# Performance work log

Hardware: AMD Instinct MI355X
Metric: run time of the kernel (lower is better)

The kernel has to match this reference:

```python
import jax, jax.numpy as jnp
import numpy as np


def setup_inputs() -> dict:
    key = jax.random.key(0)
    k1, k2, k3 = jax.random.split(key, 3)
    num, c_in, c_out, din, dout = 64, 4, 4, 2, 2
    sx = sy = 256
    nx, ny = sx // 2 + sx % 2, sy // 2 + sy % 2
    x = jax.random.normal(k1, (num, c_in, din, sx, sy), dtype=jnp.float32)
    # weight tensor: (c_in, c_out, nx, ny, din, din, din, din, dout)
    tensors = jax.random.normal(k2, (c_in, c_out, nx, ny, din, din, din, din, dout), dtype=jnp.float32)
    bias = jax.random.normal(k3, (c_out, nx, ny, dout), dtype=jnp.float32) * 1e-8
    return {"x": x, "tensors": tensors, "bias": bias}


def reference(x, tensors, bias):
    # x: (n, c, d, sx, sy); tensors: (c, p, nx, ny, d, d, d, d, o); bias: (p, nx, ny, o)
    n, c, d, sx, sy = x.shape
    nx = sx // 2 + sx % 2
    ny = sy // 2 + sy % 2
    # boundary-clamped 2x2 patch indices (matches min(2*i+1, s-1) in the source)
    ix0 = jnp.arange(nx) * 2
    ix1 = jnp.minimum(ix0 + 1, sx - 1)
    iy0 = jnp.arange(ny) * 2
    iy1 = jnp.minimum(iy0 + 1, sy - 1)
    # four corner pixels of every 2x2 patch, each (n, c, d, nx, ny)
    a = x[:, :, :, ix0][:, :, :, :, iy0]  # (2i,   2j)
    b = x[:, :, :, ix1][:, :, :, :, iy0]  # (2i+1, 2j)
    e = x[:, :, :, ix0][:, :, :, :, iy1]  # (2i,   2j+1)
    f = x[:, :, :, ix1][:, :, :, :, iy1]  # (2i+1, 2j+1)
    # outer product of the four local features -> (n, c, nx, ny, d^4)
    patch = jnp.einsum('ncixy,ncjxy,nckxy,nclxy->ncxyijkl', a, b, e, f)
    patch = patch.reshape(n, c, nx, ny, d ** 4)
    c_out, dout = tensors.shape[1], tensors.shape[-1]
    w = tensors.reshape(c, c_out, nx, ny, d ** 4, dout)
    # per-position contraction over c_in and the d^4 patch index
    out = jnp.einsum('ncxyq,cpxyqo->npoxy', patch, w)
    out = out + bias.transpose(0, 3, 1, 2)[None]  # (1, p, o, nx, ny)
    return out
```

## Files before the change

### kernel.cpp

```cpp
#include <hip/hip_runtime.h>

#define NUMN 64
#define CIN 4
#define COUT 4
#define SX 256
#define SY 256
#define NXX 128
#define NYY 128
#define YTILE 8
#define NSPLIT 2
#define NPER (NUMN / NSPLIT)

__global__ __launch_bounds__(64, 4)
void ttn_kernel(const float* __restrict__ x, const float* __restrict__ w,
                const float* __restrict__ bias, float* __restrict__ out)
{
    __shared__ float lds[2][256];

    const int bid = blockIdx.x;
    const int xi = bid % NXX;
    const int yt = (bid / NXX) % (NYY / YTILE);
    const int ns = bid / (NXX * (NYY / YTILE));

    const int tid = threadIdx.x;
    const int yl  = tid & (YTILE - 1);
    const int po  = tid >> 3;
    const int p   = po >> 1;
    const int o   = po & 1;
    const int y   = yt * YTILE + yl;

    float wr[CIN][16];
#pragma unroll
    for (int c = 0; c < CIN; ++c) {
        const float4* wp4 = (const float4*)(w +
            ((size_t)(((c * COUT + p) * NXX + xi) * NYY + y)) * 32);
#pragma unroll
        for (int j = 0; j < 8; ++j) {
            const float4 v = wp4[j];
            wr[c][2 * j]     = o ? v.y : v.x;
            wr[c][2 * j + 1] = o ? v.w : v.z;
        }
    }
    const float bv = bias[(((p * NXX + xi) * NYY + y) * 2) + o];

    const int mc   = tid >> 2;
    const int j0   = (tid & 3) * 4;
    const int prow = mc >> 1;
    const int r    = mc & 1;
    const size_t nstr = (size_t)CIN * 2 * SX * SY;
    const size_t ostr = (size_t)COUT * 2 * NXX * NYY;

    const float* xg = x + (size_t)(ns * NPER) * nstr
                        + ((size_t)prow * SX + (2 * xi + r)) * SY + yt * 16 + j0;
    float* ob = out + (size_t)(ns * NPER) * ostr
                    + (size_t)po * (NXX * NYY) + xi * NYY + y;
    float* ldsw = &lds[0][0] + tid * 4;

    float4 P0 = *(const float4*)xg;
    float4 P1 = *(const float4*)(xg + nstr);

    for (int n = 0; n < NPER; ++n) {
        const int cur = n & 1;
        *(float4*)(ldsw + cur * 256) = P0;
        P0 = P1;
        const int np = (n + 2 < NPER) ? (n + 2) : (NPER - 1);
        P1 = *(const float4*)(xg + (size_t)np * nstr);

        __syncthreads();

        const float2* l2 = (const float2*)&lds[cur][0];
        float acc = bv;
#pragma unroll
        for (int c = 0; c < CIN; ++c) {
            const float2 ae0 = l2[c * 32 +      yl];
            const float2 bf0 = l2[c * 32 +  8 + yl];
            const float2 ae1 = l2[c * 32 + 16 + yl];
            const float2 bf1 = l2[c * 32 + 24 + yl];
            const float a0 = ae0.x, e0 = ae0.y, b0 = bf0.x, f0 = bf0.y;
            const float a1 = ae1.x, e1 = ae1.y, b1 = bf1.x, f1 = bf1.y;
            const float ef00 = e0*f0, ef01 = e0*f1, ef10 = e1*f0, ef11 = e1*f1;
            const float ab00 = a0*b0, ab01 = a0*b1, ab10 = a1*b0, ab11 = a1*b1;
            const float* wq = wr[c];
            float t;
            t = ef00*wq[ 0] + ef01*wq[ 1] + ef10*wq[ 2] + ef11*wq[ 3];  acc += ab00 * t;
            t = ef00*wq[ 4] + ef01*wq[ 5] + ef10*wq[ 6] + ef11*wq[ 7];  acc += ab01 * t;
            t = ef00*wq[ 8] + ef01*wq[ 9] + ef10*wq[10] + ef11*wq[11];  acc += ab10 * t;
            t = ef00*wq[12] + ef01*wq[13] + ef10*wq[14] + ef11*wq[15];  acc += ab11 * t;
        }
        ob[(size_t)n * ostr] = acc;
    }
}

extern "C" void kernel_launch(void* const* d_in, const int* in_sizes, int n_in,
                              void* d_out, int out_size, void* d_ws, size_t ws_size,
                              hipStream_t stream) {
    const float* x    = (const float*)d_in[0];
    const float* w    = (const float*)d_in[1];
    const float* bias = (const float*)d_in[2];
    float* out = (float*)d_out;

    const int grid = NXX * (NYY / YTILE) * NSPLIT;
    ttn_kernel<<<grid, 64, 0, stream>>>(x, w, bias, out);
}
```

Baseline: 248.0 us.

## Stream x tiles directly into LDS with 4-slot async global_load_lds pipeline

Replaces register-staged double buffering of the input patch with direct global-to-LDS loads through __builtin_amdgcn_global_load_lds, using a four-slot ring that prefetches three samples ahead. The __syncthreads barrier is dropped and each wavefront instead waits on vmcnt counts, which works because the block is a single 64-thread wave. The goal is to remove the VGPR round trip and the barrier and to keep more loads in flight. In exchange, correctness depends on the hand-written vmcnt values matching the number of outstanding loads, including the interleaved output stores, and the LDS footprint doubles.

Result: faster. 236.8 us (-4.5%).

```diff
diff --git a/kernel.cpp b/kernel.cpp
--- a/kernel.cpp
+++ b/kernel.cpp
@@ -10,12 +10,13 @@
 #define YTILE 8
 #define NSPLIT 2
 #define NPER (NUMN / NSPLIT)
+#define PLANE (SX * SY)
 
 __global__ __launch_bounds__(64, 4)
 void ttn_kernel(const float* __restrict__ x, const float* __restrict__ w,
                 const float* __restrict__ bias, float* __restrict__ out)
 {
-    __shared__ float lds[2][256];
+    __shared__ float lds[4 * 256];
 
     const int bid = blockIdx.x;
     const int xi = bid % NXX;
@@ -43,39 +44,49 @@
     }
     const float bv = bias[(((p * NXX + xi) * NYY + y) * 2) + o];
 
-    const int mc   = tid >> 2;
-    const int j0   = (tid & 3) * 4;
-    const int prow = mc >> 1;
-    const int r    = mc & 1;
-    const size_t nstr = (size_t)CIN * 2 * SX * SY;
+    const size_t nstr = (size_t)CIN * 2 * PLANE;
     const size_t ostr = (size_t)COUT * 2 * NXX * NYY;
 
-    const float* xg = x + (size_t)(ns * NPER) * nstr
-                        + ((size_t)prow * SX + (2 * xi + r)) * SY + yt * 16 + j0;
+    const int mc = tid >> 2;
+    const int cd = mc >> 1;
+    const int rr = mc & 1;
+    const int j0 = (tid & 3) * 4;
+
+    const float* xs = x + (size_t)(ns * NPER) * nstr
+                        + (size_t)cd * PLANE
+                        + (size_t)(2 * xi + rr) * SY + yt * 16 + j0;
     float* ob = out + (size_t)(ns * NPER) * ostr
                     + (size_t)po * (NXX * NYY) + xi * NYY + y;
-    float* ldsw = &lds[0][0] + tid * 4;
+    float* lb = &lds[0];
 
-    float4 P0 = *(const float4*)xg;
-    float4 P1 = *(const float4*)(xg + nstr);
+    asm volatile("s_waitcnt vmcnt(0)" ::: "memory");
+
+#define STAGE(nn, slot)                                                        \
+    __builtin_amdgcn_global_load_lds(                                          \
+        (const __attribute__((address_space(1))) void*)(xs + (size_t)(nn) * nstr), \
+        (__attribute__((address_space(3))) void*)(lb + ((slot) << 8)), 16, 0, 0)
+
+    STAGE(0, 0);
+    STAGE(1, 1);
+    STAGE(2, 2);
 
     for (int n = 0; n < NPER; ++n) {
-        const int cur = n & 1;
-        *(float4*)(ldsw + cur * 256) = P0;
-        P0 = P1;
-        const int np = (n + 2 < NPER) ? (n + 2) : (NPER - 1);
-        P1 = *(const float4*)(xg + (size_t)np * nstr);
+        const int ns3 = (n + 3 < NPER) ? (n + 3) : (NPER - 1);
+        STAGE(ns3, ns3 & 3);
 
-        __syncthreads();
+        if      (n >= 3) asm volatile("s_waitcnt vmcnt(6)" ::: "memory");
+        else if (n == 2) asm volatile("s_waitcnt vmcnt(5)" ::: "memory");
+        else if (n == 1) asm volatile("s_waitcnt vmcnt(4)" ::: "memory");
+        else             asm volatile("s_waitcnt vmcnt(3)" ::: "memory");
 
-        const float2* l2 = (const float2*)&lds[cur][0];
+        const float2* b2 = (const float2*)(lb + ((n & 3) << 8));
         float acc = bv;
 #pragma unroll
         for (int c = 0; c < CIN; ++c) {
-            const float2 ae0 = l2[c * 32 +      yl];
-            const float2 bf0 = l2[c * 32 +  8 + yl];
-            const float2 ae1 = l2[c * 32 + 16 + yl];
-            const float2 bf1 = l2[c * 32 + 24 + yl];
+            const float2 ae0 = b2[c * 32 +      yl];
+            const float2 bf0 = b2[c * 32 +  8 + yl];
+            const float2 ae1 = b2[c * 32 + 16 + yl];
+            const float2 bf1 = b2[c * 32 + 24 + yl];
             const float a0 = ae0.x, e0 = ae0.y, b0 = bf0.x, f0 = bf0.y;
             const float a1 = ae1.x, e1 = ae1.y, b1 = bf1.x, f1 = bf1.y;
             const float ef00 = e0*f0, ef01 = e0*f1, ef10 = e1*f0, ef11 = e1*f1;
@@ -89,6 +100,7 @@
         }
         ob[(size_t)n * ostr] = acc;
     }
+#undef STAGE
 }
 
 extern "C" void kernel_launch(void* const* d_in, const int* in_sizes, int n_in,
```
